# Performance work log

Hardware: AMD Instinct MI355X
Metric: run time of the kernel (lower is better)

## Reference

```python
import jax, jax.numpy as jnp
import numpy as np

N = 100000       # num_nodes
E = 1600000      # num_edges (avg degree 16)
EL = 200000      # link-prediction edges
IN_C = 64
POS = 16
HID = 64
OUT = 32


def setup_inputs() -> dict:
    key = jax.random.key(0)
    ks = jax.random.split(key, 10)
    def glorot(k, shape):
        scale = 1.0 / np.sqrt(shape[0])
        return jax.random.uniform(k, shape, jnp.float32, -scale, scale)
    return {
        "x": jax.random.normal(ks[0], (N, IN_C), jnp.float32),
        "pos_emb": jax.random.normal(ks[1], (N, POS), jnp.float32),
        "W1": glorot(ks[2], (IN_C + POS, HID)),
        "b1": jnp.zeros((HID,), jnp.float32),
        "W2": glorot(ks[3], (HID, OUT)),
        "b2": jnp.zeros((OUT,), jnp.float32),
        "Wl": glorot(ks[4], (2 * OUT, 1)),
        "bl": jnp.zeros((1,), jnp.float32),
        "edge_index": jax.random.randint(ks[5], (2, E), 0, N, jnp.int32),
        "edge_label_index": jax.random.randint(ks[6], (2, EL), 0, N, jnp.int32),
    }


def reference(x, pos_emb, W1, b1, W2, b2, Wl, bl, edge_index, edge_label_index):
    n = x.shape[0]
    # GCNConv: add self-loops, symmetric deg^{-1/2} normalization (PyG defaults)
    loops = jnp.arange(n, dtype=edge_index.dtype)
    src = jnp.concatenate([edge_index[0], loops])  # [E+N]
    dst = jnp.concatenate([edge_index[1], loops])  # [E+N]
    deg = jax.ops.segment_sum(jnp.ones_like(dst, jnp.float32), dst, num_segments=n)
    dinv = jnp.where(deg > 0, jax.lax.rsqrt(jnp.maximum(deg, 1e-12)), 0.0)
    norm = dinv[src] * dinv[dst]  # [E+N]

    def gcn_conv(h, W, b):
        hw = h @ W                                    # [N, d_out] transform first
        msg = hw[src] * norm[:, None]                 # gather + normalize
        return jax.ops.segment_sum(msg, dst, num_segments=n) + b  # scatter-add

    h = jnp.concatenate([x, pos_emb], axis=1)         # [N, in+pos]
    h = jax.nn.relu(gcn_conv(h, W1, b1))              # dropout is eval no-op
    z = gcn_conv(h, W2, b2)                           # [N, out]

    s, d = edge_label_index[0], edge_label_index[1]
    zc = jnp.concatenate([z[s], z[d]], axis=1)        # [EL, 2*out]
    edge_pred = (zc @ Wl + bl)[:, 0]                  # [EL]
    return z, edge_pred
```

## Files before the change

### kernel.cpp

```cpp
#include <hip/hip_runtime.h>
#include <hip/hip_fp16.h>

#define NN 100000
#define NE 1600000
#define NEL 200000
#define TM 64
#define TM2 128

#define NBUCK 196
#define CAPB  10240
#define TPE   8192

__global__ __launch_bounds__(256) void k_part(const int* __restrict__ src,
                                              const int* __restrict__ dst,
                                              int* __restrict__ gcur,
                                              int* __restrict__ part) {
    __shared__ int hist[NBUCK];
    __shared__ int base[NBUCK];
    __shared__ int rk[NBUCK];
    int tid = threadIdx.x;
    for (int i = tid; i < NBUCK; i += 256) { hist[i] = 0; rk[i] = 0; }
    __syncthreads();
    int e0 = blockIdx.x * TPE;
    int e1 = min(e0 + TPE, NE);
    for (int e = e0 + tid; e < e1; e += 256)
        atomicAdd(&hist[dst[e] >> 9], 1);
    __syncthreads();
    for (int i = tid; i < NBUCK; i += 256)
        base[i] = i * CAPB + atomicAdd(&gcur[i], hist[i]);
    __syncthreads();
    for (int e = e0 + tid; e < e1; e += 256) {
        int d = dst[e];
        int s = src[e];
        int b = d >> 9;
        int r = atomicAdd(&rk[b], 1);
        part[base[b] + r] = ((d & 511) << 17) | s;
    }
}

__global__ __launch_bounds__(256) void k_build(const int* __restrict__ gcur,
                                               const int* __restrict__ part,
                                               int* __restrict__ csr,
                                               int* __restrict__ off,
                                               float* __restrict__ dinv) {
    __shared__ int cnts[256];
    __shared__ int hist[512];
    __shared__ int loff[512];
    __shared__ int ssum[256];
    __shared__ int csrbuf[CAPB];
    int b = blockIdx.x;
    int tid = threadIdx.x;
    cnts[tid] = (tid < NBUCK) ? gcur[tid] : 0;
    __syncthreads();
    for (int st = 1; st < 256; st <<= 1) {
        int tmp = (tid >= st) ? cnts[tid - st] : 0;
        __syncthreads();
        cnts[tid] += tmp;
        __syncthreads();
    }
    int obase = (b == 0) ? 0 : cnts[b - 1];
    int cnt = gcur[b];
    int pbase = b * CAPB;
    hist[tid] = 0; hist[tid + 256] = 0;
    __syncthreads();
    for (int i = tid; i < cnt; i += 256)
        atomicAdd(&hist[part[pbase + i] >> 17], 1);
    __syncthreads();
    int a0 = hist[2 * tid], a1 = hist[2 * tid + 1];
    int pairs = a0 + a1;
    ssum[tid] = pairs;
    __syncthreads();
    for (int st = 1; st < 256; st <<= 1) {
        int tmp = (tid >= st) ? ssum[tid - st] : 0;
        __syncthreads();
        ssum[tid] += tmp;
        __syncthreads();
    }
    int pexcl = ssum[tid] - pairs;
    loff[2 * tid] = pexcl;
    loff[2 * tid + 1] = pexcl + a0;
    __syncthreads();
    for (int i = tid; i < 512; i += 256) {
        int d = b * 512 + i;
        if (d < NN) {
            int c = hist[i];
            off[d] = obase + loff[i] + c;
            dinv[d] = rsqrtf((float)(c + 1));
        }
    }
    hist[tid] = 0; hist[tid + 256] = 0;
    __syncthreads();
    for (int i = tid; i < cnt; i += 256) {
        int rec = part[pbase + i];
        int dl = rec >> 17;
        int r = atomicAdd(&hist[dl], 1);
        csrbuf[loff[dl] + r] = rec & 0x1FFFF;
    }
    __syncthreads();
    for (int i = tid; i < cnt; i += 256)
        csr[obase + i] = csrbuf[i];
}

__global__ __launch_bounds__(256) void k_hw1(const float* __restrict__ x,
                                             const float* __restrict__ pos,
                                             const float* __restrict__ W1,
                                             const float* __restrict__ dinv,
                                             __half* __restrict__ hw1) {
    __shared__ float sh[TM * 80];
    __shared__ float sw[80 * 64];
    int tid = threadIdx.x;
    for (int t = tid; t < 80 * 64; t += 256) sw[t] = W1[t];
    int nb = blockIdx.x * TM;
    for (int i = tid; i < TM * 64; i += 256) {
        int node = i >> 6, ch = i & 63;
        int g = nb + node;
        sh[node * 80 + ch] = (g < NN) ? x[g * 64 + ch] : 0.0f;
    }
    for (int i = tid; i < TM * 16; i += 256) {
        int node = i >> 4, ch = i & 15;
        int g = nb + node;
        sh[node * 80 + 64 + ch] = (g < NN) ? pos[g * 16 + ch] : 0.0f;
    }
    __syncthreads();
    int j  = (tid & 15) * 4;
    int nl = (tid >> 4) * 4;
    float a00=0,a01=0,a02=0,a03=0, a10=0,a11=0,a12=0,a13=0;
    float a20=0,a21=0,a22=0,a23=0, a30=0,a31=0,a32=0,a33=0;
#pragma unroll 4
    for (int k = 0; k < 80; ++k) {
        float4 wv = *(const float4*)&sw[k * 64 + j];
        float h0 = sh[(nl + 0) * 80 + k];
        float h1 = sh[(nl + 1) * 80 + k];
        float h2 = sh[(nl + 2) * 80 + k];
        float h3 = sh[(nl + 3) * 80 + k];
        a00 += h0 * wv.x; a01 += h0 * wv.y; a02 += h0 * wv.z; a03 += h0 * wv.w;
        a10 += h1 * wv.x; a11 += h1 * wv.y; a12 += h1 * wv.z; a13 += h1 * wv.w;
        a20 += h2 * wv.x; a21 += h2 * wv.y; a22 += h2 * wv.z; a23 += h2 * wv.w;
        a30 += h3 * wv.x; a31 += h3 * wv.y; a32 += h3 * wv.z; a33 += h3 * wv.w;
    }
    int g0 = nb + nl;
    union { __half2 h2v[2]; float2 f2; } u;
#define STORE_ROW(r, b0, b1, b2, b3)                                          \
    if (g0 + r < NN) {                                                        \
        float sc = dinv[g0 + r];                                              \
        u.h2v[0] = __floats2half2_rn(b0 * sc, b1 * sc);                       \
        u.h2v[1] = __floats2half2_rn(b2 * sc, b3 * sc);                       \
        *(float2*)&hw1[(g0 + r) * 64 + j] = u.f2;                             \
    }
    STORE_ROW(0, a00, a01, a02, a03)
    STORE_ROW(1, a10, a11, a12, a13)
    STORE_ROW(2, a20, a21, a22, a23)
    STORE_ROW(3, a30, a31, a32, a33)
#undef STORE_ROW
}

__global__ __launch_bounds__(256) void k_gather1(const int* __restrict__ off,
                                                 const int* __restrict__ csr,
                                                 const float* __restrict__ dinv,
                                                 const __half* __restrict__ hw,
                                                 const float* __restrict__ b1,
                                                 __half* __restrict__ h2out) {
    int lane = threadIdx.x & 63;
    int wave = threadIdx.x >> 6;
    int d = blockIdx.x * 4 + wave;
    int start = (d == 0) ? 0 : off[d - 1];
    int end = off[d];
    start = __builtin_amdgcn_readfirstlane(start);
    end   = __builtin_amdgcn_readfirstlane(end);
    float dd = dinv[d];
    float hself = __half2float(hw[d * 64 + lane]);
    float acc0 = 0.0f, acc1 = 0.0f, acc2 = 0.0f, acc3 = 0.0f;
    for (int e = start; e < end; e += 16) {
        int rem = end - e;
        int s0 = csr[e];
        int s1  = (rem > 1)  ? csr[e + 1]  : s0;
        int s2  = (rem > 2)  ? csr[e + 2]  : s0;
        int s3  = (rem > 3)  ? csr[e + 3]  : s0;
        int s4  = (rem > 4)  ? csr[e + 4]  : s0;
        int s5  = (rem > 5)  ? csr[e + 5]  : s0;
        int s6  = (rem > 6)  ? csr[e + 6]  : s0;
        int s7  = (rem > 7)  ? csr[e + 7]  : s0;
        int s8  = (rem > 8)  ? csr[e + 8]  : s0;
        int s9  = (rem > 9)  ? csr[e + 9]  : s0;
        int s10 = (rem > 10) ? csr[e + 10] : s0;
        int s11 = (rem > 11) ? csr[e + 11] : s0;
        int s12 = (rem > 12) ? csr[e + 12] : s0;
        int s13 = (rem > 13) ? csr[e + 13] : s0;
        int s14 = (rem > 14) ? csr[e + 14] : s0;
        int s15 = (rem > 15) ? csr[e + 15] : s0;
        float g0  = __half2float(hw[s0  * 64 + lane]);
        float g1  = __half2float(hw[s1  * 64 + lane]);
        float g2  = __half2float(hw[s2  * 64 + lane]);
        float g3  = __half2float(hw[s3  * 64 + lane]);
        float g4  = __half2float(hw[s4  * 64 + lane]);
        float g5  = __half2float(hw[s5  * 64 + lane]);
        float g6  = __half2float(hw[s6  * 64 + lane]);
        float g7  = __half2float(hw[s7  * 64 + lane]);
        float g8  = __half2float(hw[s8  * 64 + lane]);
        float g9  = __half2float(hw[s9  * 64 + lane]);
        float g10 = __half2float(hw[s10 * 64 + lane]);
        float g11 = __half2float(hw[s11 * 64 + lane]);
        float g12 = __half2float(hw[s12 * 64 + lane]);
        float g13 = __half2float(hw[s13 * 64 + lane]);
        float g14 = __half2float(hw[s14 * 64 + lane]);
        float g15 = __half2float(hw[s15 * 64 + lane]);
        int inv = 16 - rem;
        if (inv < 0) inv = 0;
        acc0 += g0;  acc1 += g1;  acc2 += g2;  acc3 += g3;
        acc0 += g4;  acc1 += g5;  acc2 += g6;  acc3 += g7;
        acc0 += g8;  acc1 += g9;  acc2 += g10; acc3 += g11;
        acc0 += g12; acc1 += g13; acc2 += g14; acc3 += g15;
        acc3 = fmaf(-(float)inv, g0, acc3);
    }
    float v = fmaxf(b1[lane] + dd * (((acc0 + acc1) + (acc2 + acc3)) + hself), 0.0f);
    h2out[d * 64 + lane] = __float2half_rn(v);
}

__global__ __launch_bounds__(256) void k_hw2(const __half* __restrict__ h2,
                                             const float* __restrict__ W2,
                                             const float* __restrict__ dinv,
                                             __half* __restrict__ hw2) {
    __shared__ float sh[TM2 * 65];
    __shared__ float sw[64 * 32];
    int tid = threadIdx.x;
    for (int t = tid; t < 64 * 32; t += 256) sw[t] = W2[t];
    int nb = blockIdx.x * TM2;
    for (int i = tid; i < TM2 * 64; i += 256) {
        int node = i >> 6, ch = i & 63;
        int g = nb + node;
        sh[node * 65 + ch] = (g < NN) ? __half2float(h2[g * 64 + ch]) : 0.0f;
    }
    __syncthreads();
    int j  = (tid & 7) * 4;
    int nl = (tid >> 3) * 4;
    float a00=0,a01=0,a02=0,a03=0, a10=0,a11=0,a12=0,a13=0;
    float a20=0,a21=0,a22=0,a23=0, a30=0,a31=0,a32=0,a33=0;
#pragma unroll 4
    for (int k = 0; k < 64; ++k) {
        float4 wv = *(const float4*)&sw[k * 32 + j];
        float h0 = sh[(nl + 0) * 65 + k];
        float h1 = sh[(nl + 1) * 65 + k];
        float h2v = sh[(nl + 2) * 65 + k];
        float h3 = sh[(nl + 3) * 65 + k];
        a00 += h0 * wv.x;  a01 += h0 * wv.y;  a02 += h0 * wv.z;  a03 += h0 * wv.w;
        a10 += h1 * wv.x;  a11 += h1 * wv.y;  a12 += h1 * wv.z;  a13 += h1 * wv.w;
        a20 += h2v * wv.x; a21 += h2v * wv.y; a22 += h2v * wv.z; a23 += h2v * wv.w;
        a30 += h3 * wv.x;  a31 += h3 * wv.y;  a32 += h3 * wv.z;  a33 += h3 * wv.w;
    }
    int g0 = nb + nl;
    union { __half2 h2v2[2]; float2 f2; } u;
#define STORE_ROW(r, b0, b1, b2, b3)                                          \
    if (g0 + r < NN) {                                                        \
        float sc = dinv[g0 + r];                                              \
        u.h2v2[0] = __floats2half2_rn(b0 * sc, b1 * sc);                      \
        u.h2v2[1] = __floats2half2_rn(b2 * sc, b3 * sc);                      \
        *(float2*)&hw2[(g0 + r) * 32 + j] = u.f2;                            \
    }
    STORE_ROW(0, a00, a01, a02, a03)
    STORE_ROW(1, a10, a11, a12, a13)
    STORE_ROW(2, a20, a21, a22, a23)
    STORE_ROW(3, a30, a31, a32, a33)
#undef STORE_ROW
}

__global__ __launch_bounds__(256) void k_gather2(const int* __restrict__ off,
                                                 const int* __restrict__ csr,
                                                 const float* __restrict__ dinv,
                                                 const __half* __restrict__ hw,
                                                 const float* __restrict__ b2,
                                                 const float* __restrict__ Wl,
                                                 float* __restrict__ outz,
                                                 float* __restrict__ uu,
                                                 float* __restrict__ vv) {
    int lane = threadIdx.x & 63;
    int half = lane >> 5;
    int j = lane & 31;
    int wave = threadIdx.x >> 6;
    int d = blockIdx.x * 4 + wave;
    int start = (d == 0) ? 0 : off[d - 1];
    int end = off[d];
    start = __builtin_amdgcn_readfirstlane(start);
    end   = __builtin_amdgcn_readfirstlane(end);
    float dd = dinv[d];
    float hself = __half2float(hw[d * 32 + j]);
    float accA = 0.0f, accB = 0.0f, accC = 0.0f, accD = 0.0f;
    for (int e = start; e < end; e += 16) {
        int rem = end - e;
        int s0 = csr[e];
        int i1 = e + half;
        int sA = (half      < rem) ? csr[i1]      : s0;
        int sB = (half + 2  < rem) ? csr[i1 + 2]  : s0;
        int sC = (half + 4  < rem) ? csr[i1 + 4]  : s0;
        int sD = (half + 6  < rem) ? csr[i1 + 6]  : s0;
        int sE = (half + 8  < rem) ? csr[i1 + 8]  : s0;
        int sF = (half + 10 < rem) ? csr[i1 + 10] : s0;
        int sG = (half + 12 < rem) ? csr[i1 + 12] : s0;
        int sH = (half + 14 < rem) ? csr[i1 + 14] : s0;
        float gA = __half2float(hw[sA * 32 + j]);
        float gB = __half2float(hw[sB * 32 + j]);
        float gC = __half2float(hw[sC * 32 + j]);
        float gD = __half2float(hw[sD * 32 + j]);
        float gE = __half2float(hw[sE * 32 + j]);
        float gF = __half2float(hw[sF * 32 + j]);
        float gG = __half2float(hw[sG * 32 + j]);
        float gH = __half2float(hw[sH * 32 + j]);
        int nv = (rem - half + 1) >> 1;
        if (nv > 8) nv = 8;
        int inv = 8 - nv;
        accA += gA; accB += gB; accC += gC; accD += gD;
        accA += gE; accB += gF; accC += gG; accD += gH;
        accD = fmaf(-(float)inv, gH, accD);
    }
    float acc = (accA + accB) + (accC + accD);
    acc += __shfl(acc, lane ^ 32, 64);
    float z = b2[j] + dd * (acc + hself);
    if (half == 0)
        outz[d * 32 + j] = z;
    float p0 = z * Wl[j];
    float p1 = z * Wl[32 + j];
    p0 += __shfl_xor(p0, 1, 64);  p1 += __shfl_xor(p1, 1, 64);
    p0 += __shfl_xor(p0, 2, 64);  p1 += __shfl_xor(p1, 2, 64);
    p0 += __shfl_xor(p0, 4, 64);  p1 += __shfl_xor(p1, 4, 64);
    p0 += __shfl_xor(p0, 8, 64);  p1 += __shfl_xor(p1, 8, 64);
    p0 += __shfl_xor(p0, 16, 64); p1 += __shfl_xor(p1, 16, 64);
    if (lane == 0) { uu[d] = p0; vv[d] = p1; }
}

__global__ __launch_bounds__(256) void k_linkpred(const int* __restrict__ sidx,
                                                  const int* __restrict__ didx,
                                                  const float* __restrict__ uu,
                                                  const float* __restrict__ vv,
                                                  const float* __restrict__ bl,
                                                  float* __restrict__ pred) {
    int e = blockIdx.x * 256 + threadIdx.x;
    if (e < NEL)
        pred[e] = uu[sidx[e]] + vv[didx[e]] + bl[0];
}

extern "C" void kernel_launch(void* const* d_in, const int* in_sizes, int n_in,
                              void* d_out, int out_size, void* d_ws, size_t ws_size,
                              hipStream_t stream) {
    const float* x    = (const float*)d_in[0];
    const float* pos  = (const float*)d_in[1];
    const float* W1   = (const float*)d_in[2];
    const float* b1   = (const float*)d_in[3];
    const float* W2   = (const float*)d_in[4];
    const float* b2   = (const float*)d_in[5];
    const float* Wl   = (const float*)d_in[6];
    const float* bl   = (const float*)d_in[7];
    const int*   ei   = (const int*)d_in[8];
    const int*   eli  = (const int*)d_in[9];
    const int* src  = ei;
    const int* dst  = ei + NE;
    const int* lsrc = eli;
    const int* ldst = eli + NEL;

    float* out_z    = (float*)d_out;
    float* out_pred = (float*)d_out + NN * 32;

    float*  dinv  = (float*)d_ws;
    int*    off   = (int*)(dinv + NN);
    int*    gcur  = off + NN;
    int*    csr   = gcur + NBUCK;
    __half* hw1   = (__half*)(csr + NE);
    int*    part  = (int*)hw1;
    __half* h2    = hw1 + NN * 64;
    __half* hw2   = h2 + NN * 64;
    float*  uu    = (float*)h2;
    float*  vv    = uu + NN;

    hipMemsetAsync(gcur, 0, NBUCK * sizeof(int), stream);
    k_part<<<(NE + TPE - 1) / TPE, 256, 0, stream>>>(src, dst, gcur, part);
    k_build<<<NBUCK, 256, 0, stream>>>(gcur, part, csr, off, dinv);

    k_hw1<<<(NN + TM - 1) / TM, 256, 0, stream>>>(x, pos, W1, dinv, hw1);

    k_gather1<<<NN / 4, 256, 0, stream>>>(off, csr, dinv, hw1, b1, h2);

    k_hw2<<<(NN + TM2 - 1) / TM2, 256, 0, stream>>>(h2, W2, dinv, hw2);

    k_gather2<<<NN / 4, 256, 0, stream>>>(off, csr, dinv, hw2, b2, Wl,
                                          out_z, uu, vv);

    k_linkpred<<<(NEL + 255) / 256, 256, 0, stream>>>(lsrc, ldst, uu, vv, bl,
                                                      out_pred);
}
```

Before: 296.9 us.

## Compute both dense transforms with split-bf16 MFMA instead of scalar FP32 FMA

Replaces the FP32 shared-memory register-tiled GEMMs in k_hw1 and k_hw2 with bf16 MFMA 16x16x32 instructions. To keep near-FP32 accuracy, each operand is split into hi and lo bf16 parts and three cross products are accumulated. This moves the dense node transforms onto the matrix cores. The cost is extra conversion work when staging into LDS and scalar half stores, which are less coalesced than the old float2 stores.

```diff
diff --git a/kernel.cpp b/kernel.cpp
--- a/kernel.cpp
+++ b/kernel.cpp
@@ -4,12 +4,21 @@
 #define NN 100000
 #define NE 1600000
 #define NEL 200000
-#define TM 64
-#define TM2 128
 
 #define NBUCK 196
 #define CAPB  10240
 #define TPE   8192
+
+typedef short s16x8 __attribute__((ext_vector_type(8)));
+typedef float f32x4 __attribute__((ext_vector_type(4)));
+
+__device__ __forceinline__ unsigned short bf16hi(float v) {
+    unsigned u = __float_as_uint(v);
+    return (unsigned short)((u + 0x7FFFu + ((u >> 16) & 1u)) >> 16);
+}
+__device__ __forceinline__ float bf16tof(unsigned short b) {
+    return __uint_as_float(((unsigned)b) << 16);
+}
 
 __global__ __launch_bounds__(256) void k_part(const int* __restrict__ src,
                                               const int* __restrict__ dst,
@@ -101,57 +110,94 @@
         csr[obase + i] = csrbuf[i];
 }
 
+#define HW1_K 104
 __global__ __launch_bounds__(256) void k_hw1(const float* __restrict__ x,
                                              const float* __restrict__ pos,
                                              const float* __restrict__ W1,
                                              const float* __restrict__ dinv,
                                              __half* __restrict__ hw1) {
-    __shared__ float sh[TM * 80];
-    __shared__ float sw[80 * 64];
+    __shared__ unsigned short ahi[64 * HW1_K];
+    __shared__ unsigned short alo[64 * HW1_K];
+    __shared__ unsigned short bhi[64 * HW1_K];
+    __shared__ unsigned short blo[64 * HW1_K];
+    __shared__ float sdin[64];
     int tid = threadIdx.x;
-    for (int t = tid; t < 80 * 64; t += 256) sw[t] = W1[t];
-    int nb = blockIdx.x * TM;
-    for (int i = tid; i < TM * 64; i += 256) {
-        int node = i >> 6, ch = i & 63;
-        int g = nb + node;
-        sh[node * 80 + ch] = (g < NN) ? x[g * 64 + ch] : 0.0f;
-    }
-    for (int i = tid; i < TM * 16; i += 256) {
-        int node = i >> 4, ch = i & 15;
-        int g = nb + node;
-        sh[node * 80 + 64 + ch] = (g < NN) ? pos[g * 16 + ch] : 0.0f;
-    }
-    __syncthreads();
-    int j  = (tid & 15) * 4;
-    int nl = (tid >> 4) * 4;
-    float a00=0,a01=0,a02=0,a03=0, a10=0,a11=0,a12=0,a13=0;
-    float a20=0,a21=0,a22=0,a23=0, a30=0,a31=0,a32=0,a33=0;
-#pragma unroll 4
-    for (int k = 0; k < 80; ++k) {
-        float4 wv = *(const float4*)&sw[k * 64 + j];
-        float h0 = sh[(nl + 0) * 80 + k];
-        float h1 = sh[(nl + 1) * 80 + k];
-        float h2 = sh[(nl + 2) * 80 + k];
-        float h3 = sh[(nl + 3) * 80 + k];
-        a00 += h0 * wv.x; a01 += h0 * wv.y; a02 += h0 * wv.z; a03 += h0 * wv.w;
-        a10 += h1 * wv.x; a11 += h1 * wv.y; a12 += h1 * wv.z; a13 += h1 * wv.w;
-        a20 += h2 * wv.x; a21 += h2 * wv.y; a22 += h2 * wv.z; a23 += h2 * wv.w;
-        a30 += h3 * wv.x; a31 += h3 * wv.y; a32 += h3 * wv.z; a33 += h3 * wv.w;
-    }
-    int g0 = nb + nl;
-    union { __half2 h2v[2]; float2 f2; } u;
-#define STORE_ROW(r, b0, b1, b2, b3)                                          \
-    if (g0 + r < NN) {                                                        \
-        float sc = dinv[g0 + r];                                              \
-        u.h2v[0] = __floats2half2_rn(b0 * sc, b1 * sc);                       \
-        u.h2v[1] = __floats2half2_rn(b2 * sc, b3 * sc);                       \
-        *(float2*)&hw1[(g0 + r) * 64 + j] = u.f2;                             \
-    }
-    STORE_ROW(0, a00, a01, a02, a03)
-    STORE_ROW(1, a10, a11, a12, a13)
-    STORE_ROW(2, a20, a21, a22, a23)
-    STORE_ROW(3, a30, a31, a32, a33)
-#undef STORE_ROW
+    int nb = blockIdx.x * 64;
+    for (int i = tid; i < 64 * 24; i += 256) {
+        int r = i / 24, c = i - r * 24;
+        ahi[r * HW1_K + 80 + c] = 0; alo[r * HW1_K + 80 + c] = 0;
+        bhi[r * HW1_K + 80 + c] = 0; blo[r * HW1_K + 80 + c] = 0;
+    }
+    for (int i = tid; i < 64 * 64; i += 256) {
+        int r = i >> 6, c = i & 63;
+        int g = nb + r;
+        float v = (g < NN) ? x[g * 64 + c] : 0.0f;
+        unsigned short h = bf16hi(v);
+        ahi[r * HW1_K + c] = h;
+        alo[r * HW1_K + c] = bf16hi(v - bf16tof(h));
+    }
+    for (int i = tid; i < 64 * 16; i += 256) {
+        int r = i >> 4, c = i & 15;
+        int g = nb + r;
+        float v = (g < NN) ? pos[g * 16 + c] : 0.0f;
+        unsigned short h = bf16hi(v);
+        ahi[r * HW1_K + 64 + c] = h;
+        alo[r * HW1_K + 64 + c] = bf16hi(v - bf16tof(h));
+    }
+    for (int i = tid; i < 80 * 64; i += 256) {
+        int k = i >> 6, c = i & 63;
+        float v = W1[i];
+        unsigned short h = bf16hi(v);
+        bhi[c * HW1_K + k] = h;
+        blo[c * HW1_K + k] = bf16hi(v - bf16tof(h));
+    }
+    for (int i = tid; i < 64; i += 256) {
+        int g = nb + i;
+        sdin[i] = (g < NN) ? dinv[g] : 0.0f;
+    }
+    __syncthreads();
+    int wave = tid >> 6, lane = tid & 63;
+    int frow = lane & 15, fq = lane >> 4;
+    int r0 = wave * 16;
+    int aoff = (r0 + frow) * HW1_K + fq * 8;
+    s16x8 ah0 = *(s16x8*)&ahi[aoff];
+    s16x8 ah1 = *(s16x8*)&ahi[aoff + 32];
+    s16x8 ah2 = *(s16x8*)&ahi[aoff + 64];
+    s16x8 al0 = *(s16x8*)&alo[aoff];
+    s16x8 al1 = *(s16x8*)&alo[aoff + 32];
+    s16x8 al2 = *(s16x8*)&alo[aoff + 64];
+    f32x4 acc[4];
+#pragma unroll
+    for (int ct = 0; ct < 4; ++ct) {
+        acc[ct] = (f32x4)(0.0f);
+        int boff = (ct * 16 + frow) * HW1_K + fq * 8;
+        s16x8 bh0 = *(s16x8*)&bhi[boff];
+        s16x8 bh1 = *(s16x8*)&bhi[boff + 32];
+        s16x8 bh2 = *(s16x8*)&bhi[boff + 64];
+        s16x8 bl0 = *(s16x8*)&blo[boff];
+        s16x8 bl1 = *(s16x8*)&blo[boff + 32];
+        s16x8 bl2 = *(s16x8*)&blo[boff + 64];
+        acc[ct] = __builtin_amdgcn_mfma_f32_16x16x32_bf16(ah0, bh0, acc[ct], 0, 0, 0);
+        acc[ct] = __builtin_amdgcn_mfma_f32_16x16x32_bf16(ah1, bh1, acc[ct], 0, 0, 0);
+        acc[ct] = __builtin_amdgcn_mfma_f32_16x16x32_bf16(ah2, bh2, acc[ct], 0, 0, 0);
+        acc[ct] = __builtin_amdgcn_mfma_f32_16x16x32_bf16(ah0, bl0, acc[ct], 0, 0, 0);
+        acc[ct] = __builtin_amdgcn_mfma_f32_16x16x32_bf16(ah1, bl1, acc[ct], 0, 0, 0);
+        acc[ct] = __builtin_amdgcn_mfma_f32_16x16x32_bf16(ah2, bl2, acc[ct], 0, 0, 0);
+        acc[ct] = __builtin_amdgcn_mfma_f32_16x16x32_bf16(al0, bh0, acc[ct], 0, 0, 0);
+        acc[ct] = __builtin_amdgcn_mfma_f32_16x16x32_bf16(al1, bh1, acc[ct], 0, 0, 0);
+        acc[ct] = __builtin_amdgcn_mfma_f32_16x16x32_bf16(al2, bh2, acc[ct], 0, 0, 0);
+    }
+#pragma unroll
+    for (int ct = 0; ct < 4; ++ct) {
+        int col = ct * 16 + frow;
+#pragma unroll
+        for (int i = 0; i < 4; ++i) {
+            int r = r0 + fq * 4 + i;
+            int g = nb + r;
+            if (g < NN)
+                hw1[g * 64 + col] = __float2half_rn(acc[ct][i] * sdin[r]);
+        }
+    }
 }
 
 __global__ __launch_bounds__(256) void k_gather1(const int* __restrict__ off,
@@ -216,51 +262,82 @@
     h2out[d * 64 + lane] = __float2half_rn(v);
 }
 
+#define HW2_K 72
 __global__ __launch_bounds__(256) void k_hw2(const __half* __restrict__ h2,
                                              const float* __restrict__ W2,
                                              const float* __restrict__ dinv,
                                              __half* __restrict__ hw2) {
-    __shared__ float sh[TM2 * 65];
-    __shared__ float sw[64 * 32];
+    __shared__ unsigned short ahi[128 * HW2_K];
+    __shared__ unsigned short alo[128 * HW2_K];
+    __shared__ unsigned short bhi[32 * HW2_K];
+    __shared__ unsigned short blo[32 * HW2_K];
+    __shared__ float sdin[128];
     int tid = threadIdx.x;
-    for (int t = tid; t < 64 * 32; t += 256) sw[t] = W2[t];
-    int nb = blockIdx.x * TM2;
-    for (int i = tid; i < TM2 * 64; i += 256) {
-        int node = i >> 6, ch = i & 63;
-        int g = nb + node;
-        sh[node * 65 + ch] = (g < NN) ? __half2float(h2[g * 64 + ch]) : 0.0f;
-    }
-    __syncthreads();
-    int j  = (tid & 7) * 4;
-    int nl = (tid >> 3) * 4;
-    float a00=0,a01=0,a02=0,a03=0, a10=0,a11=0,a12=0,a13=0;
-    float a20=0,a21=0,a22=0,a23=0, a30=0,a31=0,a32=0,a33=0;
-#pragma unroll 4
-    for (int k = 0; k < 64; ++k) {
-        float4 wv = *(const float4*)&sw[k * 32 + j];
-        float h0 = sh[(nl + 0) * 65 + k];
-        float h1 = sh[(nl + 1) * 65 + k];
-        float h2v = sh[(nl + 2) * 65 + k];
-        float h3 = sh[(nl + 3) * 65 + k];
-        a00 += h0 * wv.x;  a01 += h0 * wv.y;  a02 += h0 * wv.z;  a03 += h0 * wv.w;
-        a10 += h1 * wv.x;  a11 += h1 * wv.y;  a12 += h1 * wv.z;  a13 += h1 * wv.w;
-        a20 += h2v * wv.x; a21 += h2v * wv.y; a22 += h2v * wv.z; a23 += h2v * wv.w;
-        a30 += h3 * wv.x;  a31 += h3 * wv.y;  a32 += h3 * wv.z;  a33 += h3 * wv.w;
-    }
-    int g0 = nb + nl;
-    union { __half2 h2v2[2]; float2 f2; } u;
-#define STORE_ROW(r, b0, b1, b2, b3)                                          \
-    if (g0 + r < NN) {                                                        \
-        float sc = dinv[g0 + r];                                              \
-        u.h2v2[0] = __floats2half2_rn(b0 * sc, b1 * sc);                      \
-        u.h2v2[1] = __floats2half2_rn(b2 * sc, b3 * sc);                      \
-        *(float2*)&hw2[(g0 + r) * 32 + j] = u.f2;                            \
-    }
-    STORE_ROW(0, a00, a01, a02, a03)
-    STORE_ROW(1, a10, a11, a12, a13)
-    STORE_ROW(2, a20, a21, a22, a23)
-    STORE_ROW(3, a30, a31, a32, a33)
-#undef STORE_ROW
+    int nb = blockIdx.x * 128;
+    for (int i = tid; i < 128 * 32; i += 256) {
+        int r = i >> 5, cp = i & 31;
+        int g = nb + r;
+        __half2 hv = (g < NN) ? ((const __half2*)h2)[g * 32 + cp]
+                              : __floats2half2_rn(0.0f, 0.0f);
+        float2 f = __half22float2(hv);
+        unsigned short h0 = bf16hi(f.x), h1 = bf16hi(f.y);
+        ahi[r * HW2_K + 2 * cp]     = h0;
+        ahi[r * HW2_K + 2 * cp + 1] = h1;
+        alo[r * HW2_K + 2 * cp]     = bf16hi(f.x - bf16tof(h0));
+        alo[r * HW2_K + 2 * cp + 1] = bf16hi(f.y - bf16tof(h1));
+    }
+    for (int i = tid; i < 64 * 32; i += 256) {
+        int k = i >> 5, c = i & 31;
+        float v = W2[i];
+        unsigned short h = bf16hi(v);
+        bhi[c * HW2_K + k] = h;
+        blo[c * HW2_K + k] = bf16hi(v - bf16tof(h));
+    }
+    for (int i = tid; i < 128; i += 256) {
+        int g = nb + i;
+        sdin[i] = (g < NN) ? dinv[g] : 0.0f;
+    }
+    __syncthreads();
+    int wave = tid >> 6, lane = tid & 63;
+    int frow = lane & 15, fq = lane >> 4;
+    int r0 = wave * 32;
+    f32x4 acc[2][2];
+#pragma unroll
+    for (int rt = 0; rt < 2; ++rt) {
+        int aoff = (r0 + rt * 16 + frow) * HW2_K + fq * 8;
+        s16x8 ah0 = *(s16x8*)&ahi[aoff];
+        s16x8 ah1 = *(s16x8*)&ahi[aoff + 32];
+        s16x8 al0 = *(s16x8*)&alo[aoff];
+        s16x8 al1 = *(s16x8*)&alo[aoff + 32];
+#pragma unroll
+        for (int ct = 0; ct < 2; ++ct) {
+            acc[rt][ct] = (f32x4)(0.0f);
+            int boff = (ct * 16 + frow) * HW2_K + fq * 8;
+            s16x8 bh0 = *(s16x8*)&bhi[boff];
+            s16x8 bh1 = *(s16x8*)&bhi[boff + 32];
+            s16x8 bl0 = *(s16x8*)&blo[boff];
+            s16x8 bl1 = *(s16x8*)&blo[boff + 32];
+            acc[rt][ct] = __builtin_amdgcn_mfma_f32_16x16x32_bf16(ah0, bh0, acc[rt][ct], 0, 0, 0);
+            acc[rt][ct] = __builtin_amdgcn_mfma_f32_16x16x32_bf16(ah1, bh1, acc[rt][ct], 0, 0, 0);
+            acc[rt][ct] = __builtin_amdgcn_mfma_f32_16x16x32_bf16(ah0, bl0, acc[rt][ct], 0, 0, 0);
+            acc[rt][ct] = __builtin_amdgcn_mfma_f32_16x16x32_bf16(ah1, bl1, acc[rt][ct], 0, 0, 0);
+            acc[rt][ct] = __builtin_amdgcn_mfma_f32_16x16x32_bf16(al0, bh0, acc[rt][ct], 0, 0, 0);
+            acc[rt][ct] = __builtin_amdgcn_mfma_f32_16x16x32_bf16(al1, bh1, acc[rt][ct], 0, 0, 0);
+        }
+    }
+#pragma unroll
+    for (int rt = 0; rt < 2; ++rt)
+#pragma unroll
+        for (int ct = 0; ct < 2; ++ct) {
+            int col = ct * 16 + frow;
+#pragma unroll
+            for (int i = 0; i < 4; ++i) {
+                int r = r0 + rt * 16 + fq * 4 + i;
+                int g = nb + r;
+                if (g < NN)
+                    hw2[g * 32 + col] = __float2half_rn(acc[rt][ct][i] * sdin[r]);
+            }
+        }
 }
 
 __global__ __launch_bounds__(256) void k_gather2(const int* __restrict__ off,
@@ -373,11 +450,11 @@
     k_part<<<(NE + TPE - 1) / TPE, 256, 0, stream>>>(src, dst, gcur, part);
     k_build<<<NBUCK, 256, 0, stream>>>(gcur, part, csr, off, dinv);
 
-    k_hw1<<<(NN + TM - 1) / TM, 256, 0, stream>>>(x, pos, W1, dinv, hw1);
+    k_hw1<<<(NN + 63) / 64, 256, 0, stream>>>(x, pos, W1, dinv, hw1);
 
     k_gather1<<<NN / 4, 256, 0, stream>>>(off, csr, dinv, hw1, b1, h2);
 
-    k_hw2<<<(NN + TM2 - 1) / TM2, 256, 0, stream>>>(h2, W2, dinv, hw2);
+    k_hw2<<<(NN + 127) / 128, 256, 0, stream>>>(h2, W2, dinv, hw2);
 
     k_gather2<<<NN / 4, 256, 0, stream>>>(off, csr, dinv, hw2, b2, Wl,
                                           out_z, uu, vv);
```

After: 290.1 us. 2.3% less time.
